# Kernel optimization log

Measured on AMD Instinct MI355X. Metric: run time of the kernel, lower is better.

Reference implementation:

```python
import jax, jax.numpy as jnp
import numpy as np

DIM = 2048
N_HEADS = 32
N_KV_HEADS = 8
HEAD_DIM = DIM // N_HEADS  # 64
SEQ = 2048
BATCH = 2


def _rope_freqs(seq_len, head_dim, theta=10000.0):
    inv = 1.0 / (theta ** (np.arange(0, head_dim, 2)[: head_dim // 2].astype(np.float32) / head_dim))
    t = np.arange(seq_len, dtype=np.float32)
    ang = np.outer(t, inv)  # (seq, head_dim//2)
    return jnp.asarray(np.cos(ang)), jnp.asarray(np.sin(ang))


def setup_inputs() -> dict:
    key = jax.random.key(0)
    ks = jax.random.split(key, 5)
    x = jax.random.normal(ks[0], (BATCH, SEQ, DIM), dtype=jnp.float32)
    s = 1.0 / np.sqrt(DIM)
    wq = jax.random.normal(ks[1], (N_HEADS * HEAD_DIM, DIM), dtype=jnp.float32) * s
    wk = jax.random.normal(ks[2], (N_KV_HEADS * HEAD_DIM, DIM), dtype=jnp.float32) * s
    wv = jax.random.normal(ks[3], (N_KV_HEADS * HEAD_DIM, DIM), dtype=jnp.float32) * s
    wo = jax.random.normal(ks[4], (DIM, N_HEADS * HEAD_DIM), dtype=jnp.float32) * s
    freqs_cos, freqs_sin = _rope_freqs(SEQ, HEAD_DIM)
    return {"x": x, "freqs_cos": freqs_cos, "freqs_sin": freqs_sin,
            "wq": wq, "wk": wk, "wv": wv, "wo": wo}


def _apply_rope(t, cos, sin):
    # t: (B, S, H, D); cos/sin: (S, D//2) broadcast to (1, S, 1, D//2)
    B, S, H, D = t.shape
    tr = t.reshape(B, S, H, D // 2, 2)
    x0, x1 = tr[..., 0], tr[..., 1]
    c = cos[None, :, None, :]
    s = sin[None, :, None, :]
    o0 = x0 * c - x1 * s
    o1 = x0 * s + x1 * c
    return jnp.stack([o0, o1], axis=-1).reshape(B, S, H, D)


def reference(x, freqs_cos, freqs_sin, wq, wk, wv, wo):
    B, S, _ = x.shape
    H, KV, D = N_HEADS, N_KV_HEADS, HEAD_DIM
    rep = H // KV
    xq = jnp.einsum('bsd,hd->bsh', x, wq).reshape(B, S, H, D)
    xk = jnp.einsum('bsd,hd->bsh', x, wk).reshape(B, S, KV, D)
    xv = jnp.einsum('bsd,hd->bsh', x, wv).reshape(B, S, KV, D)
    xq = _apply_rope(xq, freqs_cos, freqs_sin)
    xk = _apply_rope(xk, freqs_cos, freqs_sin)
    # GQA without materializing repeated K/V: group q heads as (KV, rep).
    # repeat_interleave on dim=2 maps q head h -> kv head h // rep.
    xqg = xq.reshape(B, S, KV, rep, D)
    scale = 1.0 / jnp.sqrt(jnp.float32(D))
    scores = jnp.einsum('bqkrd,bskd->bkrqs', xqg, xk) * scale  # (B,KV,rep,S,S)
    causal = jnp.tril(jnp.ones((S, S), dtype=bool))
    scores = jnp.where(causal[None, None, None], scores, jnp.float32(-jnp.inf))
    probs = jax.nn.softmax(scores, axis=-1)
    out = jnp.einsum('bkrqs,bskd->bqkrd', probs, xv)  # (B,S,KV,rep,D)
    out = out.reshape(B, S, H * D)
    return jnp.einsum('bsh,dh->bsd', out, wo)
```

## Files before the change

kernel.cpp:

```cpp
#include <hip/hip_runtime.h>

#define DIMSZ 2048
#define NH 32
#define NKV 8
#define HD 64
#define SEQLEN 2048
#define BATCH 2
#define NROWS (BATCH*SEQLEN)
#define NQKVC 3072

typedef __bf16 bf16x8 __attribute__((ext_vector_type(8)));
typedef __bf16 bf16x2 __attribute__((ext_vector_type(2)));
typedef float f32x4v __attribute__((ext_vector_type(4)));
typedef float f32x2v __attribute__((ext_vector_type(2)));
typedef float f32x16 __attribute__((ext_vector_type(16)));

__device__ __forceinline__ unsigned short f2bf(float f) {
  __bf16 h = (__bf16)f;
  union { __bf16 h; unsigned short u; } v; v.h = h; return v.u;
}
__device__ __forceinline__ unsigned int pk2bf(float lo, float hi) {
  f32x2v v; v[0] = lo; v[1] = hi;
  bf16x2 h = __builtin_convertvector(v, bf16x2);
  union { bf16x2 h; unsigned int u; } c; c.h = h; return c.u;
}
__device__ __forceinline__ float bf2f(unsigned int bits16) {
  union { unsigned int u; float f; } v; v.u = bits16 << 16; return v.f;
}
__device__ __forceinline__ int swz128(int row, int colBytes) {
  return row * 128 + (colBytes ^ ((row & 7) << 4));
}

#define GLOAD16(g, l) __builtin_amdgcn_global_load_lds( \
    (const __attribute__((address_space(1))) unsigned int*)(g), \
    (__attribute__((address_space(3))) unsigned int*)(l), 16, 0, 0)

__global__ void k_cvt_all(const float* __restrict__ x,
                          const float* __restrict__ wq, const float* __restrict__ wk,
                          const float* __restrict__ wv, const float* __restrict__ wo,
                          unsigned short* __restrict__ xb,
                          unsigned short* __restrict__ wqkvb,
                          unsigned short* __restrict__ wob) {
  int i = blockIdx.x * 256 + threadIdx.x;
  const float* s; unsigned short* d; int off;
  if (i < 2097152)      { s = x;  d = xb;    off = i; }
  else {
    int j = i - 2097152;
    if (j < 1048576)      { s = wq; d = wqkvb; off = j; }
    else if (j < 1310720) { s = wk; d = wqkvb; off = j; s = wk; off = j; }
    else if (j < 1572864) { s = wv; d = wqkvb; off = j; }
    else                  { s = wo; d = wob;   off = j - 1572864; }
    if (j >= 1048576 && j < 1310720) {  }
  }
  if (i >= 2097152) {
    int j = i - 2097152;
    if (j < 1048576)      { s = wq; off = j;            d = wqkvb; }
    else if (j < 1310720) { s = wk; off = j - 1048576;  d = wqkvb; off += 0; }
    else if (j < 1572864) { s = wv; off = j - 1310720;  d = wqkvb; }
    else                  { s = wo; off = j - 1572864;  d = wob; }
    float4 v = reinterpret_cast<const float4*>(s)[off];
    uint2 pk; pk.x = pk2bf(v.x, v.y); pk.y = pk2bf(v.z, v.w);
    int dsti = (j < 1572864) ? j : (j - 1572864);
    reinterpret_cast<uint2*>(d)[dsti] = pk;
  } else {
    float4 v = reinterpret_cast<const float4*>(x)[i];
    uint2 pk; pk.x = pk2bf(v.x, v.y); pk.y = pk2bf(v.z, v.w);
    reinterpret_cast<uint2*>(xb)[i] = pk;
  }
}

__global__ __launch_bounds__(256, 2) void k_gemm_qkv(
    const unsigned short* __restrict__ A,
    const unsigned short* __restrict__ B,
    const float* __restrict__ fc, const float* __restrict__ fs,
    unsigned short* __restrict__ Qb, unsigned short* __restrict__ Kb,
    unsigned short* __restrict__ Vt)
{
  constexpr int BK = 64, K = DIMSZ;
  __shared__ __attribute__((aligned(16))) unsigned short smA[128 * BK];
  __shared__ __attribute__((aligned(16))) unsigned short smB[128 * BK];
  const int tid = threadIdx.x;
  const int lane = tid & 63;
  const int wid = tid >> 6;
  const int lr = lane & 15, lg = lane >> 4;
  const int gx = gridDim.x;
  int lin = blockIdx.y * gx + blockIdx.x;
  const int cpx = (gx * gridDim.y) >> 3;
  lin = (lin & 7) * cpx + (lin >> 3);
  const int m0 = (lin / gx) * 128, n0 = (lin % gx) * 128;
  const int wr = (wid >> 1) * 64, wc = (wid & 1) * 64;

  f32x4v acc[4][4];
  #pragma unroll
  for (int i = 0; i < 4; i++)
    #pragma unroll
    for (int j = 0; j < 4; j++)
      acc[i][j] = f32x4v{0.f, 0.f, 0.f, 0.f};

  for (int k0 = 0; k0 < K; k0 += BK) {
    #pragma unroll
    for (int c = 0; c < 4; c++) {
      const int chunk = wid * 4 + c;
      const int idx = chunk * 64 + lane;
      const int row = idx >> 3, s = idx & 7;
      const int ks = (s ^ (row & 7)) * 8;
      GLOAD16(A + (size_t)(m0 + row) * K + k0 + ks, &smA[chunk * 512]);
      GLOAD16(B + (size_t)(n0 + row) * K + k0 + ks, &smB[chunk * 512]);
    }
    __syncthreads();
    #pragma unroll
    for (int ks = 0; ks < 2; ks++) {
      bf16x8 af[4], bfv[4];
      #pragma unroll
      for (int m = 0; m < 4; m++)
        af[m] = *reinterpret_cast<const bf16x8*>((char*)smA + swz128(wr + m * 16 + lr, ks * 64 + lg * 16));
      #pragma unroll
      for (int n = 0; n < 4; n++)
        bfv[n] = *reinterpret_cast<const bf16x8*>((char*)smB + swz128(wc + n * 16 + lr, ks * 64 + lg * 16));
      #pragma unroll
      for (int m = 0; m < 4; m++)
        #pragma unroll
        for (int n = 0; n < 4; n++)
          acc[m][n] = __builtin_amdgcn_mfma_f32_16x16x32_bf16(af[m], bfv[n], acc[m][n], 0, 0, 0);
    }
    __syncthreads();
  }
  const int bx = n0 >> 7;
  if (bx < 20) {
    const bool isQ = bx < 16;
    const float SCL = isQ ? 0.18033688011112043f : 1.0f;
    #pragma unroll
    for (int n = 0; n < 4; n++) {
      const int col = n0 + wc + n * 16 + lr;
      const int d = col & 63;
      const int i = d >> 1;
      const float sgn = (d & 1) ? 1.0f : -1.0f;
      unsigned short* dst;
      if (isQ) dst = Qb + (size_t)(col >> 6) * (SEQLEN * HD) + d;
      else     dst = Kb + (size_t)((col - 2048) >> 6) * (SEQLEN * HD) + d;
      #pragma unroll
      for (int m = 0; m < 4; m++)
        #pragma unroll
        for (int r = 0; r < 4; r++) {
          const int row = m0 + wr + m * 16 + lg * 4 + r;
          const int s = row & (SEQLEN - 1), b = row >> 11;
          const float v = acc[m][n][r];
          const float p = __shfl_xor(v, 1);
          const float c = fc[s * 32 + i], sn = fs[s * 32 + i];
          const float o = (v * c + sgn * p * sn) * SCL;
          const size_t headStride = (size_t)(isQ ? NH : NKV) * SEQLEN * HD;
          dst[(size_t)b * headStride + (size_t)s * HD] = f2bf(o);
        }
    }
  } else {
    #pragma unroll
    for (int n = 0; n < 4; n++) {
      const int col = n0 + wc + n * 16 + lr;
      const int kvh = (col - 2560) >> 6, d = col & 63;
      #pragma unroll
      for (int m = 0; m < 4; m++) {
        const int row0 = m0 + wr + m * 16 + lg * 4;
        const int s0 = row0 & (SEQLEN - 1), b = row0 >> 11;
        uint2 pk;
        pk.x = pk2bf(acc[m][n][0], acc[m][n][1]);
        pk.y = pk2bf(acc[m][n][2], acc[m][n][3]);
        *reinterpret_cast<uint2*>(
            Vt + ((size_t)((b * NKV + kvh) * HD) + d) * SEQLEN + s0) = pk;
      }
    }
  }
}

template<int OUT_BF16>
__global__ __launch_bounds__(256, 2) void k_gemm_bt(
    const unsigned short* __restrict__ A,
    const unsigned short* __restrict__ B,
    void* __restrict__ Cv, int M, int N, int K)
{
  constexpr int BK = 64;
  __shared__ __attribute__((aligned(16))) unsigned short smA[128 * BK];
  __shared__ __attribute__((aligned(16))) unsigned short smB[128 * BK];
  const int tid = threadIdx.x;
  const int lane = tid & 63;
  const int wid = tid >> 6;
  const int lr = lane & 15, lg = lane >> 4;
  const int gx = gridDim.x;
  int lin = blockIdx.y * gx + blockIdx.x;
  const int cpx = (gx * gridDim.y) >> 3;
  lin = (lin & 7) * cpx + (lin >> 3);
  const int m0 = (lin / gx) * 128, n0 = (lin % gx) * 128;
  const int wr = (wid >> 1) * 64, wc = (wid & 1) * 64;

  f32x4v acc[4][4];
  #pragma unroll
  for (int i = 0; i < 4; i++)
    #pragma unroll
    for (int j = 0; j < 4; j++)
      acc[i][j] = f32x4v{0.f, 0.f, 0.f, 0.f};

  for (int k0 = 0; k0 < K; k0 += BK) {
    #pragma unroll
    for (int c = 0; c < 4; c++) {
      const int chunk = wid * 4 + c;
      const int idx = chunk * 64 + lane;
      const int row = idx >> 3, s = idx & 7;
      const int ks = (s ^ (row & 7)) * 8;
      GLOAD16(A + (size_t)(m0 + row) * K + k0 + ks, &smA[chunk * 512]);
      GLOAD16(B + (size_t)(n0 + row) * K + k0 + ks, &smB[chunk * 512]);
    }
    __syncthreads();
    #pragma unroll
    for (int ks = 0; ks < 2; ks++) {
      bf16x8 af[4], bfv[4];
      #pragma unroll
      for (int m = 0; m < 4; m++)
        af[m] = *reinterpret_cast<const bf16x8*>((char*)smA + swz128(wr + m * 16 + lr, ks * 64 + lg * 16));
      #pragma unroll
      for (int n = 0; n < 4; n++)
        bfv[n] = *reinterpret_cast<const bf16x8*>((char*)smB + swz128(wc + n * 16 + lr, ks * 64 + lg * 16));
      #pragma unroll
      for (int m = 0; m < 4; m++)
        #pragma unroll
        for (int n = 0; n < 4; n++)
          acc[m][n] = __builtin_amdgcn_mfma_f32_16x16x32_bf16(af[m], bfv[n], acc[m][n], 0, 0, 0);
    }
    __syncthreads();
  }
  #pragma unroll
  for (int m = 0; m < 4; m++)
    #pragma unroll
    for (int n = 0; n < 4; n++)
      #pragma unroll
      for (int r = 0; r < 4; r++) {
        const size_t row = m0 + wr + m * 16 + lg * 4 + r;
        const size_t col = n0 + wc + n * 16 + lr;
        if (OUT_BF16) ((unsigned short*)Cv)[row * N + col] = f2bf(acc[m][n][r]);
        else          ((float*)Cv)[row * N + col] = acc[m][n][r];
      }
}

__global__ __launch_bounds__(256, 2) void k_attn(
    const unsigned short* __restrict__ Qg,
    const unsigned short* __restrict__ Kg,
    const unsigned short* __restrict__ Vt,
    unsigned short* __restrict__ Og)
{
  constexpr int KVB = 64;
  __shared__ __attribute__((aligned(16))) unsigned short sK0[KVB * HD];
  __shared__ __attribute__((aligned(16))) unsigned short sK1[KVB * HD];
  __shared__ __attribute__((aligned(16))) unsigned short sV0[HD * KVB];
  __shared__ __attribute__((aligned(16))) unsigned short sV1[HD * KVB];
  const int tid = threadIdx.x;
  const int lane = tid & 63, wid = tid >> 6;
  const int l31 = lane & 31, hi = lane >> 5;
  const int orig = blockIdx.x;
  const int w = (orig & 7) * 64 + (orig >> 3);
  const int kvh = w >> 6;
  const int b = (w >> 5) & 1;
  const int h = kvh * 4 + ((w >> 3) & 3);
  const int qp = w & 7;
  const unsigned short* Qp = Qg + ((size_t)(b * NH + h) * SEQLEN) * HD;
  const unsigned short* Kp = Kg + ((size_t)(b * NKV + kvh) * SEQLEN) * HD;
  const unsigned short* Vp = Vt + ((size_t)(b * NKV + kvh) * HD) * SEQLEN;

  int srow[2], scol[2];
  #pragma unroll
  for (int c = 0; c < 2; c++) {
    const int idx = (wid * 2 + c) * 64 + lane;
    srow[c] = idx >> 3;
    scol[c] = ((idx & 7) ^ (srow[c] & 7)) * 8;
  }

  for (int phase = 0; phase < 2; phase++) {
    const int qt = phase ? (15 - qp) : qp;
    const int qrow0 = qt * 128 + wid * 32;
    const int qg = qrow0 + l31;
    bf16x8 aq[4];
    #pragma unroll
    for (int ks = 0; ks < 4; ks++)
      aq[ks] = *reinterpret_cast<const bf16x8*>(Qp + (size_t)qg * HD + ks * 16 + hi * 8);

    f32x16 accO0, accO1;
    #pragma unroll
    for (int i = 0; i < 16; i++) { accO0[i] = 0.f; accO1[i] = 0.f; }
    float mrun = -3.0e38f, lrun = 0.f;

    auto compute = [&](int kv0, auto& sKb, auto& sVb) {
      if (kv0 > qrow0 + 31) return;
      f32x16 S0, S1;
      #pragma unroll
      for (int i = 0; i < 16; i++) { S0[i] = 0.f; S1[i] = 0.f; }
      __builtin_amdgcn_s_setprio(1);
      #pragma unroll
      for (int ks = 0; ks < 4; ks++) {
        bf16x8 ak0 = *reinterpret_cast<const bf16x8*>((char*)sKb + swz128(l31,      ks * 32 + hi * 16));
        bf16x8 ak1 = *reinterpret_cast<const bf16x8*>((char*)sKb + swz128(32 + l31, ks * 32 + hi * 16));
        S0 = __builtin_amdgcn_mfma_f32_32x32x16_bf16(ak0, aq[ks], S0, 0, 0, 0);
        S1 = __builtin_amdgcn_mfma_f32_32x32x16_bf16(ak1, aq[ks], S1, 0, 0, 0);
      }
      __builtin_amdgcn_s_setprio(0);
      if (kv0 + KVB - 1 > qrow0) {
        #pragma unroll
        for (int reg = 0; reg < 16; reg++) {
          const int rl = (reg & 3) + 8 * (reg >> 2) + (hi << 2);
          if (kv0 + rl > qg)      S0[reg] = -1.0e30f;
          if (kv0 + 32 + rl > qg) S1[reg] = -1.0e30f;
        }
      }
      float tm = S0[0];
      #pragma unroll
      for (int i = 1; i < 16; i++) tm = fmaxf(tm, S0[i]);
      #pragma unroll
      for (int i = 0; i < 16; i++) tm = fmaxf(tm, S1[i]);
      tm = fmaxf(tm, __shfl_xor(tm, 32));
      const float mo = mrun;
      const bool defer = __all(tm <= mo + 8.0f);
      const float mn = defer ? mo : fmaxf(mo, tm);
      #pragma unroll
      for (int i = 0; i < 16; i++) {
        S0[i] = __builtin_amdgcn_exp2f(S0[i] - mn);
        S1[i] = __builtin_amdgcn_exp2f(S1[i] - mn);
      }
      float rs = 0.f;
      #pragma unroll
      for (int i = 0; i < 16; i++) rs += S0[i] + S1[i];
      rs += __shfl_xor(rs, 32);
      if (defer) {
        lrun += rs;
      } else {
        const float sc = __builtin_amdgcn_exp2f(mo - mn);
        mrun = mn;
        lrun = lrun * sc + rs;
        #pragma unroll
        for (int reg = 0; reg < 16; reg++) {
          const int rl = (reg & 3) + 8 * (reg >> 2) + (hi << 2);
          const float scr = __shfl(sc, rl);
          accO0[reg] *= scr; accO1[reg] *= scr;
        }
      }
      __builtin_amdgcn_s_setprio(1);
      #define PVSTEP(S16, G, CB) do {                                          \
        unsigned a0 = pk2bf(S16[(G)+0], S16[(G)+1]);                           \
        unsigned a1 = pk2bf(S16[(G)+2], S16[(G)+3]);                           \
        unsigned b0 = pk2bf(S16[(G)+4], S16[(G)+5]);                           \
        unsigned b1 = pk2bf(S16[(G)+6], S16[(G)+7]);                           \
        unsigned s0 = hi ? a0 : b0, s1 = hi ? a1 : b1;                         \
        unsigned r0 = __shfl_xor((int)s0, 32), r1 = __shfl_xor((int)s1, 32);   \
        union { unsigned u[4]; bf16x8 v; } pf;                                 \
        pf.u[0] = hi ? r0 : a0; pf.u[1] = hi ? r1 : a1;                        \
        pf.u[2] = hi ? b0 : r0; pf.u[3] = hi ? b1 : r1;                        \
        bf16x8 bv0 = *reinterpret_cast<const bf16x8*>((char*)sVb + swz128(l31,      (CB))); \
        bf16x8 bv1 = *reinterpret_cast<const bf16x8*>((char*)sVb + swz128(32 + l31, (CB))); \
        accO0 = __builtin_amdgcn_mfma_f32_32x32x16_bf16(pf.v, bv0, accO0, 0, 0, 0); \
        accO1 = __builtin_amdgcn_mfma_f32_32x32x16_bf16(pf.v, bv1, accO1, 0, 0, 0); \
      } while (0)
      PVSTEP(S0, 0,  0  + hi * 16);
      PVSTEP(S0, 8,  32 + hi * 16);
      PVSTEP(S1, 0,  64 + hi * 16);
      PVSTEP(S1, 8,  96 + hi * 16);
      #undef PVSTEP
      __builtin_amdgcn_s_setprio(0);
    };

    const int nt = qt * 2 + 2;
    GLOAD16(Kp + (size_t)srow[0] * HD + scol[0], &sK0[(wid * 2 + 0) * 512]);
    GLOAD16(Kp + (size_t)srow[1] * HD + scol[1], &sK0[(wid * 2 + 1) * 512]);
    GLOAD16(Vp + (size_t)srow[0] * SEQLEN + scol[0], &sV0[(wid * 2 + 0) * 512]);
    GLOAD16(Vp + (size_t)srow[1] * SEQLEN + scol[1], &sV0[(wid * 2 + 1) * 512]);
    __syncthreads();
    for (int t = 0; t < nt; t += 2) {
      {
        const int kn = (t + 1) * KVB;
        GLOAD16(Kp + (size_t)(kn + srow[0]) * HD + scol[0], &sK1[(wid * 2 + 0) * 512]);
        GLOAD16(Kp + (size_t)(kn + srow[1]) * HD + scol[1], &sK1[(wid * 2 + 1) * 512]);
        GLOAD16(Vp + (size_t)srow[0] * SEQLEN + kn + scol[0], &sV1[(wid * 2 + 0) * 512]);
        GLOAD16(Vp + (size_t)srow[1] * SEQLEN + kn + scol[1], &sV1[(wid * 2 + 1) * 512]);
      }
      compute(t * KVB, sK0, sV0);
      __syncthreads();
      if (t + 2 < nt) {
        const int kn = (t + 2) * KVB;
        GLOAD16(Kp + (size_t)(kn + srow[0]) * HD + scol[0], &sK0[(wid * 2 + 0) * 512]);
        GLOAD16(Kp + (size_t)(kn + srow[1]) * HD + scol[1], &sK0[(wid * 2 + 1) * 512]);
        GLOAD16(Vp + (size_t)srow[0] * SEQLEN + kn + scol[0], &sV0[(wid * 2 + 0) * 512]);
        GLOAD16(Vp + (size_t)srow[1] * SEQLEN + kn + scol[1], &sV0[(wid * 2 + 1) * 512]);
      }
      compute((t + 1) * KVB, sK1, sV1);
      __syncthreads();
    }
    const float inv = 1.0f / lrun;
    #pragma unroll
    for (int reg = 0; reg < 16; reg++) {
      const int rl = (reg & 3) + 8 * (reg >> 2) + (hi << 2);
      const float invr = __shfl(inv, rl);
      const int q = qrow0 + rl;
      const size_t base = ((size_t)(b * SEQLEN + q)) * DIMSZ + h * HD;
      Og[base + l31]      = f2bf(accO0[reg] * invr);
      Og[base + 32 + l31] = f2bf(accO1[reg] * invr);
    }
  }
}

extern "C" void kernel_launch(void* const* d_in, const int* in_sizes, int n_in,
                              void* d_out, int out_size, void* d_ws, size_t ws_size,
                              hipStream_t stream)
{
  const float* x  = (const float*)d_in[0];
  const float* fc = (const float*)d_in[1];
  const float* fs = (const float*)d_in[2];
  const float* wq = (const float*)d_in[3];
  const float* wk = (const float*)d_in[4];
  const float* wv = (const float*)d_in[5];
  const float* wo = (const float*)d_in[6];
  float* out = (float*)d_out;
  char* ws = (char*)d_ws;

  unsigned short* xb    = (unsigned short*)(ws + 0);
  unsigned short* wqkvb = (unsigned short*)(ws + 16777216);
  unsigned short* wob   = (unsigned short*)(ws + 29360128);
  unsigned short* Qb    = (unsigned short*)(ws + 62914560);
  unsigned short* Kb    = (unsigned short*)(ws + 79691776);
  unsigned short* Vtb   = (unsigned short*)(ws + 83886080);
  unsigned short* attnb = (unsigned short*)(ws + 88080384);

  k_cvt_all<<<18432, 256, 0, stream>>>(x, wq, wk, wv, wo, xb, wqkvb, wob);

  dim3 g1(24, 32);
  k_gemm_qkv<<<g1, 256, 0, stream>>>(xb, wqkvb, fc, fs, Qb, Kb, Vtb);

  k_attn<<<512, 256, 0, stream>>>(Qb, Kb, Vtb, attnb);

  dim3 g2(16, 32);
  k_gemm_bt<0><<<g2, 256, 0, stream>>>(attnb, wob, out, NROWS, DIMSZ, DIMSZ);
}
```

Baseline: 171.1 us.

## Split attention blocks to one query tile each and raise occupancy

The attention kernel used to run two query tiles per block (a light one and a heavy one, paired for causal balance). It now launches 1024 blocks with one tile each, using a remapping that interleaves heavy and light tiles and groups heads sharing a KV head. Occupancy is raised from 2 to 4 blocks per SIMD group via launch bounds, and the row max and row sum now use tree reductions to shorten dependency chains. The conversion kernel's branching is also simplified. The risks are register spilling under the tighter launch bound and less even per-block work.

```diff
diff --git a/kernel.cpp b/kernel.cpp
--- a/kernel.cpp
+++ b/kernel.cpp
@@ -24,9 +24,6 @@
   bf16x2 h = __builtin_convertvector(v, bf16x2);
   union { bf16x2 h; unsigned int u; } c; c.h = h; return c.u;
 }
-__device__ __forceinline__ float bf2f(unsigned int bits16) {
-  union { unsigned int u; float f; } v; v.u = bits16 << 16; return v.f;
-}
 __device__ __forceinline__ int swz128(int row, int colBytes) {
   return row * 128 + (colBytes ^ ((row & 7) << 4));
 }
@@ -42,31 +39,15 @@
                           unsigned short* __restrict__ wqkvb,
                           unsigned short* __restrict__ wob) {
   int i = blockIdx.x * 256 + threadIdx.x;
-  const float* s; unsigned short* d; int off;
-  if (i < 2097152)      { s = x;  d = xb;    off = i; }
-  else {
-    int j = i - 2097152;
-    if (j < 1048576)      { s = wq; d = wqkvb; off = j; }
-    else if (j < 1310720) { s = wk; d = wqkvb; off = j; s = wk; off = j; }
-    else if (j < 1572864) { s = wv; d = wqkvb; off = j; }
-    else                  { s = wo; d = wob;   off = j - 1572864; }
-    if (j >= 1048576 && j < 1310720) {  }
-  }
-  if (i >= 2097152) {
-    int j = i - 2097152;
-    if (j < 1048576)      { s = wq; off = j;            d = wqkvb; }
-    else if (j < 1310720) { s = wk; off = j - 1048576;  d = wqkvb; off += 0; }
-    else if (j < 1572864) { s = wv; off = j - 1310720;  d = wqkvb; }
-    else                  { s = wo; off = j - 1572864;  d = wob; }
-    float4 v = reinterpret_cast<const float4*>(s)[off];
-    uint2 pk; pk.x = pk2bf(v.x, v.y); pk.y = pk2bf(v.z, v.w);
-    int dsti = (j < 1572864) ? j : (j - 1572864);
-    reinterpret_cast<uint2*>(d)[dsti] = pk;
-  } else {
-    float4 v = reinterpret_cast<const float4*>(x)[i];
-    uint2 pk; pk.x = pk2bf(v.x, v.y); pk.y = pk2bf(v.z, v.w);
-    reinterpret_cast<uint2*>(xb)[i] = pk;
-  }
+  const float* s; unsigned short* d; int soff, doff;
+  if (i < 2097152)        { s = x;  d = xb;    soff = i;           doff = i; }
+  else if (i < 3145728)   { s = wq; d = wqkvb; soff = i - 2097152; doff = i - 2097152; }
+  else if (i < 3407872)   { s = wk; d = wqkvb; soff = i - 3145728; doff = i - 2097152; }
+  else if (i < 3670016)   { s = wv; d = wqkvb; soff = i - 3407872; doff = i - 2097152; }
+  else                    { s = wo; d = wob;   soff = i - 3670016; doff = i - 3670016; }
+  float4 v = reinterpret_cast<const float4*>(s)[soff];
+  uint2 pk; pk.x = pk2bf(v.x, v.y); pk.y = pk2bf(v.z, v.w);
+  reinterpret_cast<uint2*>(d)[doff] = pk;
 }
 
 __global__ __launch_bounds__(256, 2) void k_gemm_qkv(
@@ -239,7 +220,7 @@
       }
 }
 
-__global__ __launch_bounds__(256, 2) void k_attn(
+__global__ __launch_bounds__(256, 4) void k_attn(
     const unsigned short* __restrict__ Qg,
     const unsigned short* __restrict__ Kg,
     const unsigned short* __restrict__ Vt,
@@ -253,151 +234,163 @@
   const int tid = threadIdx.x;
   const int lane = tid & 63, wid = tid >> 6;
   const int l31 = lane & 31, hi = lane >> 5;
-  const int orig = blockIdx.x;
-  const int w = (orig & 7) * 64 + (orig >> 3);
-  const int kvh = w >> 6;
-  const int b = (w >> 5) & 1;
-  const int h = kvh * 4 + ((w >> 3) & 3);
-  const int qp = w & 7;
+  const int g = blockIdx.x;
+  const int i = g >> 3;
+  const int r = i >> 5;
+  const int c = i & 31;
+  const int p = (g & 7) * 2 + (c >> 4);
+  const int kvh = p & 7, b = p >> 3;
+  const int h = kvh * 4 + r;
+  const int s4 = c & 15;
+  const int qt = (r & 1) ? s4 : 15 - s4;
   const unsigned short* Qp = Qg + ((size_t)(b * NH + h) * SEQLEN) * HD;
   const unsigned short* Kp = Kg + ((size_t)(b * NKV + kvh) * SEQLEN) * HD;
   const unsigned short* Vp = Vt + ((size_t)(b * NKV + kvh) * HD) * SEQLEN;
 
   int srow[2], scol[2];
   #pragma unroll
-  for (int c = 0; c < 2; c++) {
-    const int idx = (wid * 2 + c) * 64 + lane;
-    srow[c] = idx >> 3;
-    scol[c] = ((idx & 7) ^ (srow[c] & 7)) * 8;
-  }
-
-  for (int phase = 0; phase < 2; phase++) {
-    const int qt = phase ? (15 - qp) : qp;
-    const int qrow0 = qt * 128 + wid * 32;
-    const int qg = qrow0 + l31;
-    bf16x8 aq[4];
-    #pragma unroll
-    for (int ks = 0; ks < 4; ks++)
-      aq[ks] = *reinterpret_cast<const bf16x8*>(Qp + (size_t)qg * HD + ks * 16 + hi * 8);
-
-    f32x16 accO0, accO1;
-    #pragma unroll
-    for (int i = 0; i < 16; i++) { accO0[i] = 0.f; accO1[i] = 0.f; }
-    float mrun = -3.0e38f, lrun = 0.f;
-
-    auto compute = [&](int kv0, auto& sKb, auto& sVb) {
-      if (kv0 > qrow0 + 31) return;
-      f32x16 S0, S1;
-      #pragma unroll
-      for (int i = 0; i < 16; i++) { S0[i] = 0.f; S1[i] = 0.f; }
-      __builtin_amdgcn_s_setprio(1);
-      #pragma unroll
-      for (int ks = 0; ks < 4; ks++) {
-        bf16x8 ak0 = *reinterpret_cast<const bf16x8*>((char*)sKb + swz128(l31,      ks * 32 + hi * 16));
-        bf16x8 ak1 = *reinterpret_cast<const bf16x8*>((char*)sKb + swz128(32 + l31, ks * 32 + hi * 16));
-        S0 = __builtin_amdgcn_mfma_f32_32x32x16_bf16(ak0, aq[ks], S0, 0, 0, 0);
-        S1 = __builtin_amdgcn_mfma_f32_32x32x16_bf16(ak1, aq[ks], S1, 0, 0, 0);
+  for (int cc = 0; cc < 2; cc++) {
+    const int idx = (wid * 2 + cc) * 64 + lane;
+    srow[cc] = idx >> 3;
+    scol[cc] = ((idx & 7) ^ (srow[cc] & 7)) * 8;
+  }
+
+  const int qrow0 = qt * 128 + wid * 32;
+  const int qg = qrow0 + l31;
+  bf16x8 aq[4];
+  #pragma unroll
+  for (int ks = 0; ks < 4; ks++)
+    aq[ks] = *reinterpret_cast<const bf16x8*>(Qp + (size_t)qg * HD + ks * 16 + hi * 8);
+
+  f32x16 accO0, accO1;
+  #pragma unroll
+  for (int ii = 0; ii < 16; ii++) { accO0[ii] = 0.f; accO1[ii] = 0.f; }
+  float mrun = -3.0e38f, lrun = 0.f;
+
+  auto compute = [&](int kv0, auto& sKb, auto& sVb) {
+    if (kv0 > qrow0 + 31) return;
+    f32x16 S0, S1;
+    #pragma unroll
+    for (int ii = 0; ii < 16; ii++) { S0[ii] = 0.f; S1[ii] = 0.f; }
+    __builtin_amdgcn_s_setprio(1);
+    #pragma unroll
+    for (int ks = 0; ks < 4; ks++) {
+      bf16x8 ak0 = *reinterpret_cast<const bf16x8*>((char*)sKb + swz128(l31,      ks * 32 + hi * 16));
+      bf16x8 ak1 = *reinterpret_cast<const bf16x8*>((char*)sKb + swz128(32 + l31, ks * 32 + hi * 16));
+      S0 = __builtin_amdgcn_mfma_f32_32x32x16_bf16(ak0, aq[ks], S0, 0, 0, 0);
+      S1 = __builtin_amdgcn_mfma_f32_32x32x16_bf16(ak1, aq[ks], S1, 0, 0, 0);
+    }
+    __builtin_amdgcn_s_setprio(0);
+    if (kv0 + KVB - 1 > qrow0) {
+      #pragma unroll
+      for (int reg = 0; reg < 16; reg++) {
+        const int rl = (reg & 3) + 8 * (reg >> 2) + (hi << 2);
+        if (kv0 + rl > qg)      S0[reg] = -1.0e30f;
+        if (kv0 + 32 + rl > qg) S1[reg] = -1.0e30f;
       }
-      __builtin_amdgcn_s_setprio(0);
-      if (kv0 + KVB - 1 > qrow0) {
-        #pragma unroll
-        for (int reg = 0; reg < 16; reg++) {
-          const int rl = (reg & 3) + 8 * (reg >> 2) + (hi << 2);
-          if (kv0 + rl > qg)      S0[reg] = -1.0e30f;
-          if (kv0 + 32 + rl > qg) S1[reg] = -1.0e30f;
-        }
+    }
+    float t16[16];
+    #pragma unroll
+    for (int ii = 0; ii < 16; ii++) t16[ii] = fmaxf(S0[ii], S1[ii]);
+    float t8[8];
+    #pragma unroll
+    for (int ii = 0; ii < 8; ii++) t8[ii] = fmaxf(t16[ii], t16[ii + 8]);
+    float t4[4];
+    #pragma unroll
+    for (int ii = 0; ii < 4; ii++) t4[ii] = fmaxf(t8[ii], t8[ii + 4]);
+    float tm = fmaxf(fmaxf(t4[0], t4[1]), fmaxf(t4[2], t4[3]));
+    tm = fmaxf(tm, __shfl_xor(tm, 32));
+    const float mo = mrun;
+    const bool defer = __all(tm <= mo + 8.0f);
+    const float mn = defer ? mo : fmaxf(mo, tm);
+    #pragma unroll
+    for (int ii = 0; ii < 16; ii++) {
+      S0[ii] = __builtin_amdgcn_exp2f(S0[ii] - mn);
+      S1[ii] = __builtin_amdgcn_exp2f(S1[ii] - mn);
+    }
+    float u16[16];
+    #pragma unroll
+    for (int ii = 0; ii < 16; ii++) u16[ii] = S0[ii] + S1[ii];
+    float u8[8];
+    #pragma unroll
+    for (int ii = 0; ii < 8; ii++) u8[ii] = u16[ii] + u16[ii + 8];
+    float u4[4];
+    #pragma unroll
+    for (int ii = 0; ii < 4; ii++) u4[ii] = u8[ii] + u8[ii + 4];
+    float rs = (u4[0] + u4[1]) + (u4[2] + u4[3]);
+    rs += __shfl_xor(rs, 32);
+    if (defer) {
+      lrun += rs;
+    } else {
+      const float sc = __builtin_amdgcn_exp2f(mo - mn);
+      mrun = mn;
+      lrun = lrun * sc + rs;
+      #pragma unroll
+      for (int reg = 0; reg < 16; reg++) {
+        const int rl = (reg & 3) + 8 * (reg >> 2) + (hi << 2);
+        const float scr = __shfl(sc, rl);
+        accO0[reg] *= scr; accO1[reg] *= scr;
       }
-      float tm = S0[0];
-      #pragma unroll
-      for (int i = 1; i < 16; i++) tm = fmaxf(tm, S0[i]);
-      #pragma unroll
-      for (int i = 0; i < 16; i++) tm = fmaxf(tm, S1[i]);
-      tm = fmaxf(tm, __shfl_xor(tm, 32));
-      const float mo = mrun;
-      const bool defer = __all(tm <= mo + 8.0f);
-      const float mn = defer ? mo : fmaxf(mo, tm);
-      #pragma unroll
-      for (int i = 0; i < 16; i++) {
-        S0[i] = __builtin_amdgcn_exp2f(S0[i] - mn);
-        S1[i] = __builtin_amdgcn_exp2f(S1[i] - mn);
-      }
-      float rs = 0.f;
-      #pragma unroll
-      for (int i = 0; i < 16; i++) rs += S0[i] + S1[i];
-      rs += __shfl_xor(rs, 32);
-      if (defer) {
-        lrun += rs;
-      } else {
-        const float sc = __builtin_amdgcn_exp2f(mo - mn);
-        mrun = mn;
-        lrun = lrun * sc + rs;
-        #pragma unroll
-        for (int reg = 0; reg < 16; reg++) {
-          const int rl = (reg & 3) + 8 * (reg >> 2) + (hi << 2);
-          const float scr = __shfl(sc, rl);
-          accO0[reg] *= scr; accO1[reg] *= scr;
-        }
-      }
-      __builtin_amdgcn_s_setprio(1);
-      #define PVSTEP(S16, G, CB) do {                                          \
-        unsigned a0 = pk2bf(S16[(G)+0], S16[(G)+1]);                           \
-        unsigned a1 = pk2bf(S16[(G)+2], S16[(G)+3]);                           \
-        unsigned b0 = pk2bf(S16[(G)+4], S16[(G)+5]);                           \
-        unsigned b1 = pk2bf(S16[(G)+6], S16[(G)+7]);                           \
-        unsigned s0 = hi ? a0 : b0, s1 = hi ? a1 : b1;                         \
-        unsigned r0 = __shfl_xor((int)s0, 32), r1 = __shfl_xor((int)s1, 32);   \
-        union { unsigned u[4]; bf16x8 v; } pf;                                 \
-        pf.u[0] = hi ? r0 : a0; pf.u[1] = hi ? r1 : a1;                        \
-        pf.u[2] = hi ? b0 : r0; pf.u[3] = hi ? b1 : r1;                        \
-        bf16x8 bv0 = *reinterpret_cast<const bf16x8*>((char*)sVb + swz128(l31,      (CB))); \
-        bf16x8 bv1 = *reinterpret_cast<const bf16x8*>((char*)sVb + swz128(32 + l31, (CB))); \
-        accO0 = __builtin_amdgcn_mfma_f32_32x32x16_bf16(pf.v, bv0, accO0, 0, 0, 0); \
-        accO1 = __builtin_amdgcn_mfma_f32_32x32x16_bf16(pf.v, bv1, accO1, 0, 0, 0); \
-      } while (0)
-      PVSTEP(S0, 0,  0  + hi * 16);
-      PVSTEP(S0, 8,  32 + hi * 16);
-      PVSTEP(S1, 0,  64 + hi * 16);
-      PVSTEP(S1, 8,  96 + hi * 16);
-      #undef PVSTEP
-      __builtin_amdgcn_s_setprio(0);
-    };
-
-    const int nt = qt * 2 + 2;
-    GLOAD16(Kp + (size_t)srow[0] * HD + scol[0], &sK0[(wid * 2 + 0) * 512]);
-    GLOAD16(Kp + (size_t)srow[1] * HD + scol[1], &sK0[(wid * 2 + 1) * 512]);
-    GLOAD16(Vp + (size_t)srow[0] * SEQLEN + scol[0], &sV0[(wid * 2 + 0) * 512]);
-    GLOAD16(Vp + (size_t)srow[1] * SEQLEN + scol[1], &sV0[(wid * 2 + 1) * 512]);
-    __syncthreads();
-    for (int t = 0; t < nt; t += 2) {
-      {
-        const int kn = (t + 1) * KVB;
-        GLOAD16(Kp + (size_t)(kn + srow[0]) * HD + scol[0], &sK1[(wid * 2 + 0) * 512]);
-        GLOAD16(Kp + (size_t)(kn + srow[1]) * HD + scol[1], &sK1[(wid * 2 + 1) * 512]);
-        GLOAD16(Vp + (size_t)srow[0] * SEQLEN + kn + scol[0], &sV1[(wid * 2 + 0) * 512]);
-        GLOAD16(Vp + (size_t)srow[1] * SEQLEN + kn + scol[1], &sV1[(wid * 2 + 1) * 512]);
-      }
-      compute(t * KVB, sK0, sV0);
-      __syncthreads();
-      if (t + 2 < nt) {
-        const int kn = (t + 2) * KVB;
-        GLOAD16(Kp + (size_t)(kn + srow[0]) * HD + scol[0], &sK0[(wid * 2 + 0) * 512]);
-        GLOAD16(Kp + (size_t)(kn + srow[1]) * HD + scol[1], &sK0[(wid * 2 + 1) * 512]);
-        GLOAD16(Vp + (size_t)srow[0] * SEQLEN + kn + scol[0], &sV0[(wid * 2 + 0) * 512]);
-        GLOAD16(Vp + (size_t)srow[1] * SEQLEN + kn + scol[1], &sV0[(wid * 2 + 1) * 512]);
-      }
-      compute((t + 1) * KVB, sK1, sV1);
-      __syncthreads();
-    }
-    const float inv = 1.0f / lrun;
-    #pragma unroll
-    for (int reg = 0; reg < 16; reg++) {
-      const int rl = (reg & 3) + 8 * (reg >> 2) + (hi << 2);
-      const float invr = __shfl(inv, rl);
-      const int q = qrow0 + rl;
-      const size_t base = ((size_t)(b * SEQLEN + q)) * DIMSZ + h * HD;
-      Og[base + l31]      = f2bf(accO0[reg] * invr);
-      Og[base + 32 + l31] = f2bf(accO1[reg] * invr);
-    }
+    }
+    __builtin_amdgcn_s_setprio(1);
+    #define PVSTEP(S16, G, CB) do {                                          \
+      unsigned a0 = pk2bf(S16[(G)+0], S16[(G)+1]);                           \
+      unsigned a1 = pk2bf(S16[(G)+2], S16[(G)+3]);                           \
+      unsigned b0 = pk2bf(S16[(G)+4], S16[(G)+5]);                           \
+      unsigned b1 = pk2bf(S16[(G)+6], S16[(G)+7]);                           \
+      unsigned s0 = hi ? a0 : b0, s1 = hi ? a1 : b1;                         \
+      unsigned r0 = __shfl_xor((int)s0, 32), r1 = __shfl_xor((int)s1, 32);   \
+      union { unsigned u[4]; bf16x8 v; } pf;                                 \
+      pf.u[0] = hi ? r0 : a0; pf.u[1] = hi ? r1 : a1;                        \
+      pf.u[2] = hi ? b0 : r0; pf.u[3] = hi ? b1 : r1;                        \
+      bf16x8 bv0 = *reinterpret_cast<const bf16x8*>((char*)sVb + swz128(l31,      (CB))); \
+      bf16x8 bv1 = *reinterpret_cast<const bf16x8*>((char*)sVb + swz128(32 + l31, (CB))); \
+      accO0 = __builtin_amdgcn_mfma_f32_32x32x16_bf16(pf.v, bv0, accO0, 0, 0, 0); \
+      accO1 = __builtin_amdgcn_mfma_f32_32x32x16_bf16(pf.v, bv1, accO1, 0, 0, 0); \
+    } while (0)
+    PVSTEP(S0, 0,  0  + hi * 16);
+    PVSTEP(S0, 8,  32 + hi * 16);
+    PVSTEP(S1, 0,  64 + hi * 16);
+    PVSTEP(S1, 8,  96 + hi * 16);
+    #undef PVSTEP
+    __builtin_amdgcn_s_setprio(0);
+  };
+
+  const int nt = qt * 2 + 2;
+  GLOAD16(Kp + (size_t)srow[0] * HD + scol[0], &sK0[(wid * 2 + 0) * 512]);
+  GLOAD16(Kp + (size_t)srow[1] * HD + scol[1], &sK0[(wid * 2 + 1) * 512]);
+  GLOAD16(Vp + (size_t)srow[0] * SEQLEN + scol[0], &sV0[(wid * 2 + 0) * 512]);
+  GLOAD16(Vp + (size_t)srow[1] * SEQLEN + scol[1], &sV0[(wid * 2 + 1) * 512]);
+  __syncthreads();
+  for (int t = 0; t < nt; t += 2) {
+    {
+      const int kn = (t + 1) * KVB;
+      GLOAD16(Kp + (size_t)(kn + srow[0]) * HD + scol[0], &sK1[(wid * 2 + 0) * 512]);
+      GLOAD16(Kp + (size_t)(kn + srow[1]) * HD + scol[1], &sK1[(wid * 2 + 1) * 512]);
+      GLOAD16(Vp + (size_t)srow[0] * SEQLEN + kn + scol[0], &sV1[(wid * 2 + 0) * 512]);
+      GLOAD16(Vp + (size_t)srow[1] * SEQLEN + kn + scol[1], &sV1[(wid * 2 + 1) * 512]);
+    }
+    compute(t * KVB, sK0, sV0);
+    __syncthreads();
+    if (t + 2 < nt) {
+      const int kn = (t + 2) * KVB;
+      GLOAD16(Kp + (size_t)(kn + srow[0]) * HD + scol[0], &sK0[(wid * 2 + 0) * 512]);
+      GLOAD16(Kp + (size_t)(kn + srow[1]) * HD + scol[1], &sK0[(wid * 2 + 1) * 512]);
+      GLOAD16(Vp + (size_t)srow[0] * SEQLEN + kn + scol[0], &sV0[(wid * 2 + 0) * 512]);
+      GLOAD16(Vp + (size_t)srow[1] * SEQLEN + kn + scol[1], &sV0[(wid * 2 + 1) * 512]);
+    }
+    compute((t + 1) * KVB, sK1, sV1);
+    __syncthreads();
+  }
+  const float inv = 1.0f / lrun;
+  #pragma unroll
+  for (int reg = 0; reg < 16; reg++) {
+    const int rl = (reg & 3) + 8 * (reg >> 2) + (hi << 2);
+    const float invr = __shfl(inv, rl);
+    const int q = qrow0 + rl;
+    const size_t base = ((size_t)(b * SEQLEN + q)) * DIMSZ + h * HD;
+    Og[base + l31]      = f2bf(accO0[reg] * invr);
+    Og[base + 32 + l31] = f2bf(accO1[reg] * invr);
   }
 }
 
@@ -428,7 +421,7 @@
   dim3 g1(24, 32);
   k_gemm_qkv<<<g1, 256, 0, stream>>>(xb, wqkvb, fc, fs, Qb, Kb, Vtb);
 
-  k_attn<<<512, 256, 0, stream>>>(Qb, Kb, Vtb, attnb);
+  k_attn<<<1024, 256, 0, stream>>>(Qb, Kb, Vtb, attnb);
 
   dim3 g2(16, 32);
   k_gemm_bt<0><<<g2, 256, 0, stream>>>(attnb, wob, out, NROWS, DIMSZ, DIMSZ);
```

After: 183.4 us. 7.2% more time.
